# Kernel optimization log

Measured on AMD Instinct MI355X. Metric: run time of the kernel, lower is better.

The kernel has to match this reference:

```python
import jax, jax.numpy as jnp
import numpy as np

D = 4          # subsample stride for quantized refs
R = 6          # local search radius
P = 2 * R + 1  # 13
N = P * P      # 169
C = 32         # one-hot classes
BETA = 50.0
SIG = 1.0      # gaussian kernel sigma for kernel_soft_argmax
MPR = 12       # memory_patch_R
MPP = 2 * MPR + 1  # 25
DIL_INT = 15


def bilinear_gather(img, ys, xs):
    # img (b,c,h,w); ys,xs (b,n,h,w) float pixel coords; zero padding outside.
    b, c, h, w = img.shape
    y0f = jnp.floor(ys); x0f = jnp.floor(xs)
    wy = ys - y0f; wx = xs - x0f
    y0 = y0f.astype(jnp.int32); x0 = x0f.astype(jnp.int32)
    imgf = img.reshape(b, c, h * w)

    def corner(yi, xi, wgt):
        valid = (yi >= 0) & (yi < h) & (xi >= 0) & (xi < w)
        idx = jnp.clip(yi, 0, h - 1) * w + jnp.clip(xi, 0, w - 1)  # (b,n,h,w)
        g = jax.vmap(lambda f, ix: f[:, ix])(imgf, idx)            # (b,c,n,h,w)
        return g * (wgt * valid)[:, None]

    return (corner(y0, x0, (1 - wy) * (1 - wx))
            + corner(y0, x0 + 1, (1 - wy) * wx)
            + corner(y0 + 1, x0, wy * (1 - wx))
            + corner(y0 + 1, x0 + 1, wy * wx))


def deform_im2col(img, offset):
    # img (b,c,h,w); offset (b,h,w,2) ordered (dx,dy); returns (b,c,N,h,w)
    b, c, h, w = img.shape
    n = jnp.arange(N)
    dy = (n // P - R).astype(jnp.float32)
    dx = (n % P - R).astype(jnp.float32)
    yy = jnp.arange(h, dtype=jnp.float32)[:, None]
    xx = jnp.arange(w, dtype=jnp.float32)[None, :]
    ys = yy[None, None] + offset[..., 1][:, None] + dy[None, :, None, None]
    xs = xx[None, None] + offset[..., 0][:, None] + dx[None, :, None, None]
    return bilinear_gather(img, ys, xs)


def local_corr(t, r, rad, dil):
    # SpatialCorrelationSampler(kernel_size=1, patch_size=2*rad+1, dilation_patch=dil)
    pad = rad * dil
    rp = jnp.pad(r, ((0, 0), (0, 0), (pad, pad), (pad, pad)))
    offs = jnp.arange(2 * rad + 1) * dil

    def dot(oy, ox):
        rs = jax.lax.dynamic_slice(rp, (0, 0, oy, ox), t.shape)
        return jnp.sum(t * rs, axis=1)  # (b,h,w)

    f = jax.vmap(lambda oy: jax.vmap(lambda ox: dot(oy, ox))(offs))(offs)  # (Pp,Pp,b,h,w)
    return jnp.transpose(f, (2, 0, 1, 3, 4))  # (b,Pp,Pp,h,w), axis1=dy, axis2=dx


def unfold(x, ksz, pad):
    # torch F.unfold: (b,c,h,w) -> (b,c,ksz*ksz,h*w), n = ky*ksz+kx, zero pad
    b, c, h, w = x.shape
    xp = jnp.pad(x, ((0, 0), (0, 0), (pad, pad), (pad, pad)))
    offs = jnp.arange(ksz)
    sl = jax.vmap(lambda oy: jax.vmap(
        lambda ox: jax.lax.dynamic_slice(xp, (0, 0, oy, ox), x.shape))(offs))(offs)
    return jnp.transpose(sl, (2, 3, 0, 1, 4, 5)).reshape(b, c, ksz * ksz, h * w)


def kernel_soft_argmax(corr):
    # corr (B, N, h, w): gaussian-weight then softmax(beta * .) over N
    k = jnp.arange(P, dtype=jnp.float32)
    ctr = (P - 1) / 2.0
    g = jnp.exp(-(((k[None, :] - ctr) ** 2) + ((k[:, None] - ctr) ** 2)) / (2 * SIG ** 2))
    return jax.nn.softmax(BETA * (g.reshape(1, N, 1, 1) * corr), axis=1)


def get_grid(corr):
    # corr (B, N, h, w) -> soft-argmax grid (B, h, w, 2) in normalized coords
    B, n, h, w = corr.shape
    # replicate the torch meshgrid variable swap in the original get_grid
    x_map = jnp.broadcast_to(jnp.linspace(-1.0, 1.0, w)[None, :], (h, w)).astype(jnp.float32)
    y_map = jnp.broadcast_to(jnp.linspace(-1.0, 1.0, h)[:, None], (h, w)).astype(jnp.float32)
    xg = unfold(x_map[None, None], P, R)[:, 0]  # (1,N,hw)
    yg = unfold(y_map[None, None], P, R)[:, 0]
    wgt = corr.reshape(B, n, h * w)
    wgt = wgt / jnp.sum(wgt, 1, keepdims=True)
    gx = (wgt * xg).sum(1).reshape(B, h, w, 1)
    gy = (wgt * yg).sum(1).reshape(B, h, w, 1)
    return jnp.concatenate([gx, gy], 3)


def forward(feats_r, feats_t, quantized_r, ref_index, current_ind):
    ref_list = [int(v) for v in np.asarray(ref_index)]  # static config
    cur = int(current_ind)
    nref = feats_r.shape[0]
    nsearch = len([x for x in ref_list if cur - x > DIL_INT])
    dirates = [min(4, (cur - x) // DIL_INT + 1) for x in ref_list if cur - x > DIL_INT]
    b, c, h, w = feats_t.shape

    mdy = jnp.arange(-MPR, MPR + 1, dtype=jnp.float32)
    corrs, offsets = [], []
    for si in range(nsearch):
        cc = local_corr(feats_t, feats_r[si], MPR, dirates[si])       # (b,25,25,h,w)
        cc = jax.nn.softmax(cc.reshape(b, MPP * MPP, h * w), axis=1)
        cc = cc.reshape(b, MPP, MPP, h, w)
        offx = jnp.einsum('bpqhw,q->bhw', cc, mdy)   # expectation of dx
        offy = jnp.einsum('bpqhw,p->bhw', cc, mdy)   # expectation of dy
        off = jnp.stack([offx, offy], -1) * float(dirates[si])        # (b,h,w,2)
        offsets.append(off)
        col0 = deform_im2col(feats_r[si], off)                        # (b,c,N,h,w)
        corrs.append(jnp.einsum('bchw,bcnhw->bnhw', feats_t, col0))
    for ind in range(nsearch, nref):
        corrs.append(local_corr(feats_t, feats_r[ind], R, 1).reshape(b, N, h, w))

    corr = jnp.concatenate(corrs, 0)                 # (b*nref, N, h, w)
    corr = kernel_soft_argmax(corr)
    corr = corr.reshape(b, 1, N * nref, h * w)
    grid = get_grid(corr.reshape(-1, N, h, w))       # (b*nref, h, w, 2)

    # prep: subsample ::D and one-hot single-channel label maps
    labels = quantized_r[:, :, 0, ::D, ::D]          # (nref, b, h, w)
    qr = (labels[:, :, None] == jnp.arange(C)[None, None, :, None, None]).astype(jnp.float32)

    cols = []
    for i in range(nsearch):
        cols.append(deform_im2col(qr[i], offsets[i]).reshape(b, C, N, h * w))
    for i in range(nsearch, nref):
        cols.append(unfold(qr[i], P, R))
    image_uf = jnp.concatenate(cols, 2)              # (b, C, N*nref, hw)

    out = jnp.einsum('bnl,bcnl->bcl', corr[:, 0], image_uf).reshape(b, C, h, w)
    return out, grid


def setup_inputs() -> dict:
    key = jax.random.key(0)
    k1, k2, k3 = jax.random.split(key, 3)
    feats_r = jax.random.normal(k1, (3, 1, 64, 64, 64), dtype=jnp.float32)
    feats_t = jax.random.normal(k2, (1, 64, 64, 64), dtype=jnp.float32)
    quantized_r = jax.random.randint(k3, (3, 1, 1, 256, 256), 0, C, dtype=jnp.int32)
    return {
        'feats_r': feats_r,
        'feats_t': feats_t,
        'quantized_r': quantized_r,
        'ref_index': np.arange(3),
        'current_ind': 16,
    }


def reference(feats_r, feats_t, quantized_r, ref_index, current_ind):
    return forward(feats_r, feats_t, quantized_r, ref_index, current_ind)
```

## Files before the change

kernel.cpp:

```cpp
#include <hip/hip_runtime.h>


#define NPIX 4096

typedef float f32x2 __attribute__((ext_vector_type(2)));

__device__ __forceinline__ f32x2 pkfma(f32x2 a, f32x2 b, f32x2 c) {
  f32x2 d;
  asm("v_pk_fma_f32 %0, %1, %2, %3" : "=v"(d) : "v"(a), "v"(b), "v"(c));
  return d;
}

__device__ __forceinline__ f32x2 pdot8p(float4 t0, float4 t1, float4 a,
                                        float4 b, f32x2 acc) {
  f32x2 t0l = {t0.x, t0.y}, t0h = {t0.z, t0.w};
  f32x2 t1l = {t1.x, t1.y}, t1h = {t1.z, t1.w};
  f32x2 al = {a.x, a.y}, ah = {a.z, a.w};
  f32x2 bl = {b.x, b.y}, bh = {b.z, b.w};
  acc = pkfma(t0l, al, acc);
  acc = pkfma(t0h, ah, acc);
  acc = pkfma(t1l, bl, acc);
  acc = pkfma(t1h, bh, acc);
  return acc;
}

__device__ __forceinline__ float red8_8(float p0, float p1, float p2,
                                        float p3, float p4, float p5,
                                        float p6, float p7, int tx) {
  bool o1 = tx & 1, o2 = tx & 2, o4 = tx & 4;
  float a = (o1 ? p1 : p0) + __shfl_xor(o1 ? p0 : p1, 1);
  float b = (o1 ? p3 : p2) + __shfl_xor(o1 ? p2 : p3, 1);
  float c = (o1 ? p5 : p4) + __shfl_xor(o1 ? p4 : p5, 1);
  float d = (o1 ? p7 : p6) + __shfl_xor(o1 ? p6 : p7, 1);
  float e = (o2 ? b : a) + __shfl_xor(o2 ? a : b, 2);
  float f = (o2 ? d : c) + __shfl_xor(o2 ? c : d, 2);
  return (o4 ? f : e) + __shfl_xor(o4 ? e : f, 4);
}

__device__ __forceinline__ float red8(float v) {
  v += __shfl_xor(v, 1);
  v += __shfl_xor(v, 2);
  v += __shfl_xor(v, 4);
  return v;
}

__device__ __forceinline__ float wredmax(float v) {
#pragma unroll
  for (int o = 32; o; o >>= 1) v = fmaxf(v, __shfl_down(v, o));
  return __shfl(v, 0);
}
__device__ __forceinline__ float wredsum(float v) {
#pragma unroll
  for (int o = 32; o; o >>= 1) v += __shfl_down(v, o);
  return __shfl(v, 0);
}

__global__ __launch_bounds__(256) void k_transpose(
    const float* __restrict__ ft, const float* __restrict__ fr,
    const int* __restrict__ q, float* __restrict__ tT, float* __restrict__ rT,
    unsigned char* __restrict__ lblp) {
  __shared__ float tile[64][65];
  int img = blockIdx.y;
  int pixBase = blockIdx.x * 64;
  const float* src = (img == 0) ? ft : fr + (img - 1) * (64 * NPIX);
  float* dst = (img == 0) ? tT : rT + (img - 1) * (64 * NPIX);
  int tid = threadIdx.x;
#pragma unroll
  for (int it = 0; it < 4; ++it) {
    int idx = it * 256 + tid;
    int c = idx >> 4;
    int p4 = (idx & 15) << 2;
    float4 v = *(const float4*)&src[c * NPIX + pixBase + p4];
    tile[p4 + 0][c] = v.x;
    tile[p4 + 1][c] = v.y;
    tile[p4 + 2][c] = v.z;
    tile[p4 + 3][c] = v.w;
  }
  __syncthreads();
#pragma unroll
  for (int it = 0; it < 4; ++it) {
    int idx = it * 256 + tid;
    int p = idx >> 4;
    int c4 = (idx & 15) << 2;
    float4 v = make_float4(tile[p][c4], tile[p][c4 + 1], tile[p][c4 + 2],
                           tile[p][c4 + 3]);
    *(float4*)&dst[(pixBase + p) * 64 + c4] = v;
  }
  if (img >= 1 && tid < 64) {
    int pix = pixBase + tid;
    lblp[(img - 1) * 4096 + pix] = (unsigned char)
        q[(img - 1) * 65536 + (pix >> 6) * 1024 + (pix & 63) * 4];
  }
}

__global__ __launch_bounds__(512, 4) void k_fused(
    const float* __restrict__ tT, const float* __restrict__ rT,
    const unsigned char* __restrict__ lblp, float* __restrict__ out,
    float* __restrict__ grid) {
  int xg = blockIdx.x, y = blockIdx.y;
  int x0 = (xg >> 1) * 16 + (xg & 1);
  int tid = threadIdx.x;
  int g8 = tid >> 3, tx = tid & 7;
  int w = tid >> 6, lane = tid & 63;

  __shared__ float cc1[8 * 636];
  __shared__ float D[8][196];
  __shared__ float P0[8][169];
  __shared__ float cc2[8][169];
  __shared__ float bins[8][33];

  if (tid < 264) ((float*)bins)[tid] = 0.f;

  const f32x2 zz = {0.f, 0.f};

  const float4* tb = (const float4*)&tT[((y << 6) + x0) << 6];
  float4 t0a = tb[0 * 32 + 2 * tx], t0b = tb[0 * 32 + 2 * tx + 1];
  float4 t1a = tb[1 * 32 + 2 * tx], t1b = tb[1 * 32 + 2 * tx + 1];
  float4 t2a = tb[2 * 32 + 2 * tx], t2b = tb[2 * 32 + 2 * tx + 1];
  float4 t3a = tb[3 * 32 + 2 * tx], t3b = tb[3 * 32 + 2 * tx + 1];
  float4 t4a = tb[4 * 32 + 2 * tx], t4b = tb[4 * 32 + 2 * tx + 1];
  float4 t5a = tb[5 * 32 + 2 * tx], t5b = tb[5 * 32 + 2 * tx + 1];
  float4 t6a = tb[6 * 32 + 2 * tx], t6b = tb[6 * 32 + 2 * tx + 1];
  float4 t7a = tb[7 * 32 + 2 * tx], t7b = tb[7 * 32 + 2 * tx + 1];

  {
    int u = g8 & 31, oyb = g8 >> 5;
    int rx = x0 - 24 + 2 * u;
    bool cok = (unsigned)rx < 64u;
    int colB = min(max(rx, 0), 63) * 64 + tx * 8;
    int ox = u - tx;
    bool sok = (unsigned)ox < 25u;
#pragma unroll 4
    for (int r = 0; r < 13; ++r) {
      int oy = oyb + 2 * r;
      int ry = y + 2 * oy - 24;
      bool ok = cok & (oy < 25) & ((unsigned)ry < 64u);
      const float4* rp = (const float4*)&rT[min(max(ry, 0), 63) * 4096 + colB];
      float4 ra = rp[0], rb = rp[1];
      f32x2 a0 = pdot8p(t0a, t0b, ra, rb, zz);
      f32x2 a1 = pdot8p(t1a, t1b, ra, rb, zz);
      f32x2 a2 = pdot8p(t2a, t2b, ra, rb, zz);
      f32x2 a3 = pdot8p(t3a, t3b, ra, rb, zz);
      f32x2 a4 = pdot8p(t4a, t4b, ra, rb, zz);
      f32x2 a5 = pdot8p(t5a, t5b, ra, rb, zz);
      f32x2 a6 = pdot8p(t6a, t6b, ra, rb, zz);
      f32x2 a7 = pdot8p(t7a, t7b, ra, rb, zz);
      float v = red8_8(a0.x + a0.y, a1.x + a1.y, a2.x + a2.y, a3.x + a3.y,
                       a4.x + a4.y, a5.x + a5.y, a6.x + a6.y, a7.x + a7.y,
                       tx);
      v = ok ? v : 0.f;
      if (sok && (oy < 25)) cc1[tx * 636 + oy * 25 + ox] = v;
    }
  }
  __syncthreads();

  float offx, offy;
  {
    float vv[10];
    float m = -3e38f;
#pragma unroll
    for (int it = 0; it < 10; ++it) {
      unsigned o = lane + (it << 6);
      float v = (o < 625u) ? cc1[w * 636 + o] : -3e38f;
      vv[it] = v;
      m = fmaxf(m, v);
    }
    m = wredmax(m);
    float s = 0.f, sx = 0.f, sy = 0.f;
#pragma unroll
    for (int it = 0; it < 10; ++it) {
      unsigned o = lane + (it << 6);
      unsigned oy = o / 25u, ox = o - oy * 25u;
      float e = __expf(vv[it] - m);
      s += e;
      sx += e * (float)((int)ox - 12);
      sy += e * (float)((int)oy - 12);
    }
    s = wredsum(s);
    sx = wredsum(sx);
    sy = wredsum(sy);
    offx = 2.f * sx / s;
    offy = 2.f * sy / s;
  }

  float fy = floorf(offy), fx = floorf(offx);
  float wy = offy - fy, wx = offx - fx;
  float w00 = (1.f - wy) * (1.f - wx), w01 = (1.f - wy) * wx;
  float w10 = wy * (1.f - wx), w11 = wy * wx;
  int iy0 = y + (int)fy - 6;
  int ix0 = x0 + 2 * w + (int)fx - 6;

  {
    const float4* Tp = (const float4*)&tT[((y << 6) + x0 + 2 * w) << 6];
    float4 T0 = Tp[2 * tx], T1 = Tp[2 * tx + 1];
    int g3 = lane >> 3;
#pragma unroll 4
    for (int r = 0; r < 28; ++r) {
      int idx = g3 + (r << 3);
      int a = idx >> 4, b = idx & 15;
      int ry = iy0 + a, rx = ix0 + b;
      bool ok = (b < 14) & ((unsigned)ry < 64u) & ((unsigned)rx < 64u);
      const float4* rp = (const float4*)
          &rT[(min(max(ry, 0), 63) * 64 + min(max(rx, 0), 63)) * 64];
      float4 ra = rp[2 * tx], rb = rp[2 * tx + 1];
      f32x2 acc = pdot8p(T0, T1, ra, rb, zz);
      float v = red8(acc.x + acc.y);
      if (tx == 0 && b < 14) D[w][a * 14 + b] = ok ? v : 0.f;
    }
  }

  {
    int px = x0 + 2 * w, pix = (y << 6) + px;
    float sc[3];
    float m = -3e38f;
#pragma unroll
    for (int it = 0; it < 3; ++it) {
      unsigned o = lane + (it << 6);
      float scv = -3e38f;
      if (o < 169u) {
        unsigned i = o / 13u, j = o - i * 13u;
        float v = w00 * D[w][i * 14 + j] + w01 * D[w][i * 14 + j + 1] +
                  w10 * D[w][(i + 1) * 14 + j] +
                  w11 * D[w][(i + 1) * 14 + j + 1];
        float di = (float)(((int)i - 6) * ((int)i - 6) +
                           ((int)j - 6) * ((int)j - 6));
        scv = 50.f * __expf(-0.5f * di) * v;
      }
      sc[it] = scv;
      m = fmaxf(m, scv);
    }
    m = wredmax(m);
    float ee[3];
    float s = 0.f, gx = 0.f, gy = 0.f;
#pragma unroll
    for (int it = 0; it < 3; ++it) {
      unsigned o = lane + (it << 6);
      unsigned i = o / 13u, j = o - i * 13u;
      float e = __expf(sc[it] - m);
      ee[it] = e;
      int yy = y + (int)i - 6, xx = px + (int)j - 6;
      bool inb = (o < 169u) && (unsigned)yy < 64u && (unsigned)xx < 64u;
      s += e;
      gx += e * (inb ? (-1.f + (2.f / 63.f) * (float)xx) : 0.f);
      gy += e * (inb ? (-1.f + (2.f / 63.f) * (float)yy) : 0.f);
    }
    s = wredsum(s);
    gx = wredsum(gx);
    gy = wredsum(gy);
    float invS = 1.f / s;
#pragma unroll
    for (int it = 0; it < 3; ++it) {
      unsigned o = lane + (it << 6);
      if (o < 169u) P0[w][o] = ee[it] * invS;
    }
    if (lane == 0) {
      grid[pix * 2 + 0] = gx * invS;
      grid[pix * 2 + 1] = gy * invS;
    }
  }

  {
#pragma unroll
    for (int it = 0; it < 4; ++it) {
      int idx = lane + (it << 6);
      int a = idx >> 4, b = idx & 15;
      if (a < 14 && b < 14) {
        int ry = iy0 + a, rx = ix0 + b;
        if ((unsigned)ry < 64u && (unsigned)rx < 64u) {
          float wgt = 0.f;
          const float* crp = P0[w];
          if (a < 13) {
            if (b < 13) wgt = fmaf(w00, crp[a * 13 + b], wgt);
            if (b > 0) wgt = fmaf(w01, crp[a * 13 + b - 1], wgt);
          }
          if (a > 0) {
            if (b < 13) wgt = fmaf(w10, crp[(a - 1) * 13 + b], wgt);
            if (b > 0) wgt = fmaf(w11, crp[(a - 1) * 13 + b - 1], wgt);
          }
          if (wgt != 0.f) atomicAdd(&bins[w][lblp[ry * 64 + rx]], wgt);
        }
      }
    }
  }

#pragma unroll 1
  for (int k = 1; k <= 2; ++k) {
    const float* rb0 = rT + (k << 18);
    __syncthreads();
    {
      int u = g8 & 31, ib = g8 >> 5;
      int rx = x0 - 6 + u;
      bool cok = (unsigned)rx < 64u;
      int colB = min(max(rx, 0), 63) * 64 + tx * 8;
      int j = u - 2 * tx;
      bool sok = (unsigned)j < 13u;
#pragma unroll 4
      for (int r = 0; r < 7; ++r) {
        int i = ib + 2 * r;
        int ry = y + i - 6;
        bool ok = cok & (i < 13) & ((unsigned)ry < 64u);
        const float4* rp =
            (const float4*)&rb0[min(max(ry, 0), 63) * 4096 + colB];
        float4 ra = rp[0], rb = rp[1];
        f32x2 a0 = pdot8p(t0a, t0b, ra, rb, zz);
        f32x2 a1 = pdot8p(t1a, t1b, ra, rb, zz);
        f32x2 a2 = pdot8p(t2a, t2b, ra, rb, zz);
        f32x2 a3 = pdot8p(t3a, t3b, ra, rb, zz);
        f32x2 a4 = pdot8p(t4a, t4b, ra, rb, zz);
        f32x2 a5 = pdot8p(t5a, t5b, ra, rb, zz);
        f32x2 a6 = pdot8p(t6a, t6b, ra, rb, zz);
        f32x2 a7 = pdot8p(t7a, t7b, ra, rb, zz);
        float v = red8_8(a0.x + a0.y, a1.x + a1.y, a2.x + a2.y, a3.x + a3.y,
                         a4.x + a4.y, a5.x + a5.y, a6.x + a6.y, a7.x + a7.y,
                         tx);
        v = ok ? v : 0.f;
        if (sok && (i < 13)) cc2[tx][i * 13 + j] = v;
      }
    }
    __syncthreads();
    {
      int px = x0 + 2 * w, pix = (y << 6) + px;
      float sc[3];
      float m = -3e38f;
#pragma unroll
      for (int it = 0; it < 3; ++it) {
        unsigned o = lane + (it << 6);
        float scv = -3e38f;
        if (o < 169u) {
          unsigned i = o / 13u, j = o - i * 13u;
          float di = (float)(((int)i - 6) * ((int)i - 6) +
                             ((int)j - 6) * ((int)j - 6));
          scv = 50.f * __expf(-0.5f * di) * cc2[w][o];
        }
        sc[it] = scv;
        m = fmaxf(m, scv);
      }
      m = wredmax(m);
      float ee[3];
      float s = 0.f, gx = 0.f, gy = 0.f;
#pragma unroll
      for (int it = 0; it < 3; ++it) {
        unsigned o = lane + (it << 6);
        unsigned i = o / 13u, j = o - i * 13u;
        float e = __expf(sc[it] - m);
        ee[it] = e;
        int yy = y + (int)i - 6, xx = px + (int)j - 6;
        bool inb = (o < 169u) && (unsigned)yy < 64u && (unsigned)xx < 64u;
        s += e;
        gx += e * (inb ? (-1.f + (2.f / 63.f) * (float)xx) : 0.f);
        gy += e * (inb ? (-1.f + (2.f / 63.f) * (float)yy) : 0.f);
      }
      s = wredsum(s);
      gx = wredsum(gx);
      gy = wredsum(gy);
      float invS = 1.f / s;
#pragma unroll
      for (int it = 0; it < 3; ++it) {
        unsigned o = lane + (it << 6);
        if (o < 169u) {
          unsigned i = o / 13u, j = o - i * 13u;
          int yy = y + (int)i - 6, xx = px + (int)j - 6;
          if ((unsigned)yy < 64u && (unsigned)xx < 64u)
            atomicAdd(&bins[w][lblp[(k << 12) + yy * 64 + xx]],
                      ee[it] * invS);
        }
      }
      if (lane == 0) {
        grid[(k * NPIX + pix) * 2 + 0] = gx * invS;
        grid[(k * NPIX + pix) * 2 + 1] = gy * invS;
      }
    }
    __syncthreads();
  }

  if (tid < 256) {
    int pp = tid & 7, c = tid >> 3;
    out[c * NPIX + (y << 6) + x0 + 2 * pp] = bins[pp][c];
  }
}

extern "C" void kernel_launch(void* const* d_in, const int* in_sizes, int n_in,
                              void* d_out, int out_size, void* d_ws,
                              size_t ws_size, hipStream_t stream) {
  const float* fr = (const float*)d_in[0];
  const float* ft = (const float*)d_in[1];
  const int* q = (const int*)d_in[2];
  float* out = (float*)d_out;
  float* grid = out + 32 * NPIX;

  float* ws = (float*)d_ws;
  float* tT = ws;
  float* rT = ws + 262144;
  unsigned char* lblp = (unsigned char*)(ws + 1048576);

  k_transpose<<<dim3(64, 4), 256, 0, stream>>>(ft, fr, q, tT, rT, lblp);
  k_fused<<<dim3(8, 64), 512, 0, stream>>>(tT, rT, lblp, out, grid);
}
```

Measured before the change: 55.40 us.

## Split reference frames across grid z-dimension and merge bins with global atomics

The fused kernel now launches a 3-deep grid in z so that the deformable search frame and the two local-window frames run in separate blocks instead of sequentially inside one block. Per-block class bins are combined with atomicAdd into an output buffer that is zeroed by a memset first. The cc2 buffer now aliases cc1 to cut shared memory, and the packed v_pk_fma inline asm is replaced by plain scalar fmaf dot products. This trades three times the blocks, a memset and global atomics for shorter per-block serial work, at the cost of a load imbalance because the z=0 blocks do more work than the others.

Measured after the change: 61.45 us. +10.9%, slower.

```diff
diff --git a/kernel.cpp b/kernel.cpp
--- a/kernel.cpp
+++ b/kernel.cpp
@@ -3,25 +3,14 @@
 
 #define NPIX 4096
 
-typedef float f32x2 __attribute__((ext_vector_type(2)));
-
-__device__ __forceinline__ f32x2 pkfma(f32x2 a, f32x2 b, f32x2 c) {
-  f32x2 d;
-  asm("v_pk_fma_f32 %0, %1, %2, %3" : "=v"(d) : "v"(a), "v"(b), "v"(c));
-  return d;
-}
-
-__device__ __forceinline__ f32x2 pdot8p(float4 t0, float4 t1, float4 a,
-                                        float4 b, f32x2 acc) {
-  f32x2 t0l = {t0.x, t0.y}, t0h = {t0.z, t0.w};
-  f32x2 t1l = {t1.x, t1.y}, t1h = {t1.z, t1.w};
-  f32x2 al = {a.x, a.y}, ah = {a.z, a.w};
-  f32x2 bl = {b.x, b.y}, bh = {b.z, b.w};
-  acc = pkfma(t0l, al, acc);
-  acc = pkfma(t0h, ah, acc);
-  acc = pkfma(t1l, bl, acc);
-  acc = pkfma(t1h, bh, acc);
-  return acc;
+__device__ __forceinline__ float pdot8(float4 t0, float4 t1, float4 a,
+                                       float4 b) {
+  float s0 = t0.x * a.x, s1 = t0.y * a.y, s2 = t0.z * a.z, s3 = t0.w * a.w;
+  s0 = fmaf(t1.x, b.x, s0);
+  s1 = fmaf(t1.y, b.y, s1);
+  s2 = fmaf(t1.z, b.z, s2);
+  s3 = fmaf(t1.w, b.w, s3);
+  return (s0 + s1) + (s2 + s3);
 }
 
 __device__ __forceinline__ float red8_8(float p0, float p1, float p2,
@@ -97,7 +86,7 @@
     const float* __restrict__ tT, const float* __restrict__ rT,
     const unsigned char* __restrict__ lblp, float* __restrict__ out,
     float* __restrict__ grid) {
-  int xg = blockIdx.x, y = blockIdx.y;
+  int xg = blockIdx.x, y = blockIdx.y, z = blockIdx.z;
   int x0 = (xg >> 1) * 16 + (xg & 1);
   int tid = threadIdx.x;
   int g8 = tid >> 3, tx = tid & 7;
@@ -106,12 +95,9 @@
   __shared__ float cc1[8 * 636];
   __shared__ float D[8][196];
   __shared__ float P0[8][169];
-  __shared__ float cc2[8][169];
   __shared__ float bins[8][33];
 
   if (tid < 264) ((float*)bins)[tid] = 0.f;
-
-  const f32x2 zz = {0.f, 0.f};
 
   const float4* tb = (const float4*)&tT[((y << 6) + x0) << 6];
   float4 t0a = tb[0 * 32 + 2 * tx], t0b = tb[0 * 32 + 2 * tx + 1];
@@ -123,170 +109,165 @@
   float4 t6a = tb[6 * 32 + 2 * tx], t6b = tb[6 * 32 + 2 * tx + 1];
   float4 t7a = tb[7 * 32 + 2 * tx], t7b = tb[7 * 32 + 2 * tx + 1];
 
-  {
-    int u = g8 & 31, oyb = g8 >> 5;
-    int rx = x0 - 24 + 2 * u;
-    bool cok = (unsigned)rx < 64u;
-    int colB = min(max(rx, 0), 63) * 64 + tx * 8;
-    int ox = u - tx;
-    bool sok = (unsigned)ox < 25u;
+  if (z == 0) {
+    {
+      int u = g8 & 31, oyb = g8 >> 5;
+      int rx = x0 - 24 + 2 * u;
+      bool cok = (unsigned)rx < 64u;
+      int colB = min(max(rx, 0), 63) * 64 + tx * 8;
+      int ox = u - tx;
+      bool sok = (unsigned)ox < 25u;
 #pragma unroll 4
-    for (int r = 0; r < 13; ++r) {
-      int oy = oyb + 2 * r;
-      int ry = y + 2 * oy - 24;
-      bool ok = cok & (oy < 25) & ((unsigned)ry < 64u);
-      const float4* rp = (const float4*)&rT[min(max(ry, 0), 63) * 4096 + colB];
-      float4 ra = rp[0], rb = rp[1];
-      f32x2 a0 = pdot8p(t0a, t0b, ra, rb, zz);
-      f32x2 a1 = pdot8p(t1a, t1b, ra, rb, zz);
-      f32x2 a2 = pdot8p(t2a, t2b, ra, rb, zz);
-      f32x2 a3 = pdot8p(t3a, t3b, ra, rb, zz);
-      f32x2 a4 = pdot8p(t4a, t4b, ra, rb, zz);
-      f32x2 a5 = pdot8p(t5a, t5b, ra, rb, zz);
-      f32x2 a6 = pdot8p(t6a, t6b, ra, rb, zz);
-      f32x2 a7 = pdot8p(t7a, t7b, ra, rb, zz);
-      float v = red8_8(a0.x + a0.y, a1.x + a1.y, a2.x + a2.y, a3.x + a3.y,
-                       a4.x + a4.y, a5.x + a5.y, a6.x + a6.y, a7.x + a7.y,
-                       tx);
-      v = ok ? v : 0.f;
-      if (sok && (oy < 25)) cc1[tx * 636 + oy * 25 + ox] = v;
-    }
-  }
-  __syncthreads();
-
-  float offx, offy;
-  {
-    float vv[10];
-    float m = -3e38f;
-#pragma unroll
-    for (int it = 0; it < 10; ++it) {
-      unsigned o = lane + (it << 6);
-      float v = (o < 625u) ? cc1[w * 636 + o] : -3e38f;
-      vv[it] = v;
-      m = fmaxf(m, v);
-    }
-    m = wredmax(m);
-    float s = 0.f, sx = 0.f, sy = 0.f;
-#pragma unroll
-    for (int it = 0; it < 10; ++it) {
-      unsigned o = lane + (it << 6);
-      unsigned oy = o / 25u, ox = o - oy * 25u;
-      float e = __expf(vv[it] - m);
-      s += e;
-      sx += e * (float)((int)ox - 12);
-      sy += e * (float)((int)oy - 12);
-    }
-    s = wredsum(s);
-    sx = wredsum(sx);
-    sy = wredsum(sy);
-    offx = 2.f * sx / s;
-    offy = 2.f * sy / s;
-  }
-
-  float fy = floorf(offy), fx = floorf(offx);
-  float wy = offy - fy, wx = offx - fx;
-  float w00 = (1.f - wy) * (1.f - wx), w01 = (1.f - wy) * wx;
-  float w10 = wy * (1.f - wx), w11 = wy * wx;
-  int iy0 = y + (int)fy - 6;
-  int ix0 = x0 + 2 * w + (int)fx - 6;
-
-  {
-    const float4* Tp = (const float4*)&tT[((y << 6) + x0 + 2 * w) << 6];
-    float4 T0 = Tp[2 * tx], T1 = Tp[2 * tx + 1];
-    int g3 = lane >> 3;
+      for (int r = 0; r < 13; ++r) {
+        int oy = oyb + 2 * r;
+        int ry = y + 2 * oy - 24;
+        bool ok = cok & (oy < 25) & ((unsigned)ry < 64u);
+        const float4* rp =
+            (const float4*)&rT[min(max(ry, 0), 63) * 4096 + colB];
+        float4 ra = rp[0], rb = rp[1];
+        float v = red8_8(pdot8(t0a, t0b, ra, rb), pdot8(t1a, t1b, ra, rb),
+                         pdot8(t2a, t2b, ra, rb), pdot8(t3a, t3b, ra, rb),
+                         pdot8(t4a, t4b, ra, rb), pdot8(t5a, t5b, ra, rb),
+                         pdot8(t6a, t6b, ra, rb), pdot8(t7a, t7b, ra, rb),
+                         tx);
+        v = ok ? v : 0.f;
+        if (sok && (oy < 25)) cc1[tx * 636 + oy * 25 + ox] = v;
+      }
+    }
+    __syncthreads();
+
+    float offx, offy;
+    {
+      float vv[10];
+      float m = -3e38f;
+#pragma unroll
+      for (int it = 0; it < 10; ++it) {
+        unsigned o = lane + (it << 6);
+        float v = (o < 625u) ? cc1[w * 636 + o] : -3e38f;
+        vv[it] = v;
+        m = fmaxf(m, v);
+      }
+      m = wredmax(m);
+      float s = 0.f, sx = 0.f, sy = 0.f;
+#pragma unroll
+      for (int it = 0; it < 10; ++it) {
+        unsigned o = lane + (it << 6);
+        unsigned oy = o / 25u, ox = o - oy * 25u;
+        float e = __expf(vv[it] - m);
+        s += e;
+        sx += e * (float)((int)ox - 12);
+        sy += e * (float)((int)oy - 12);
+      }
+      s = wredsum(s);
+      sx = wredsum(sx);
+      sy = wredsum(sy);
+      offx = 2.f * sx / s;
+      offy = 2.f * sy / s;
+    }
+
+    float fy = floorf(offy), fx = floorf(offx);
+    float wy = offy - fy, wx = offx - fx;
+    float w00 = (1.f - wy) * (1.f - wx), w01 = (1.f - wy) * wx;
+    float w10 = wy * (1.f - wx), w11 = wy * wx;
+    int iy0 = y + (int)fy - 6;
+    int ix0 = x0 + 2 * w + (int)fx - 6;
+
+    {
+      const float4* Tp = (const float4*)&tT[((y << 6) + x0 + 2 * w) << 6];
+      float4 T0 = Tp[2 * tx], T1 = Tp[2 * tx + 1];
+      int g3 = lane >> 3;
 #pragma unroll 4
-    for (int r = 0; r < 28; ++r) {
-      int idx = g3 + (r << 3);
-      int a = idx >> 4, b = idx & 15;
-      int ry = iy0 + a, rx = ix0 + b;
-      bool ok = (b < 14) & ((unsigned)ry < 64u) & ((unsigned)rx < 64u);
-      const float4* rp = (const float4*)
-          &rT[(min(max(ry, 0), 63) * 64 + min(max(rx, 0), 63)) * 64];
-      float4 ra = rp[2 * tx], rb = rp[2 * tx + 1];
-      f32x2 acc = pdot8p(T0, T1, ra, rb, zz);
-      float v = red8(acc.x + acc.y);
-      if (tx == 0 && b < 14) D[w][a * 14 + b] = ok ? v : 0.f;
-    }
-  }
-
-  {
-    int px = x0 + 2 * w, pix = (y << 6) + px;
-    float sc[3];
-    float m = -3e38f;
-#pragma unroll
-    for (int it = 0; it < 3; ++it) {
-      unsigned o = lane + (it << 6);
-      float scv = -3e38f;
-      if (o < 169u) {
+      for (int r = 0; r < 28; ++r) {
+        int idx = g3 + (r << 3);
+        int a = idx >> 4, b = idx & 15;
+        int ry = iy0 + a, rx = ix0 + b;
+        bool ok = (b < 14) & ((unsigned)ry < 64u) & ((unsigned)rx < 64u);
+        const float4* rp = (const float4*)
+            &rT[(min(max(ry, 0), 63) * 64 + min(max(rx, 0), 63)) * 64];
+        float4 ra = rp[2 * tx], rb = rp[2 * tx + 1];
+        float v = red8(pdot8(T0, T1, ra, rb));
+        if (tx == 0 && b < 14) D[w][a * 14 + b] = ok ? v : 0.f;
+      }
+    }
+
+    {
+      int px = x0 + 2 * w, pix = (y << 6) + px;
+      float sc[3];
+      float m = -3e38f;
+#pragma unroll
+      for (int it = 0; it < 3; ++it) {
+        unsigned o = lane + (it << 6);
+        float scv = -3e38f;
+        if (o < 169u) {
+          unsigned i = o / 13u, j = o - i * 13u;
+          float v = w00 * D[w][i * 14 + j] + w01 * D[w][i * 14 + j + 1] +
+                    w10 * D[w][(i + 1) * 14 + j] +
+                    w11 * D[w][(i + 1) * 14 + j + 1];
+          float di = (float)(((int)i - 6) * ((int)i - 6) +
+                             ((int)j - 6) * ((int)j - 6));
+          scv = 50.f * __expf(-0.5f * di) * v;
+        }
+        sc[it] = scv;
+        m = fmaxf(m, scv);
+      }
+      m = wredmax(m);
+      float ee[3];
+      float s = 0.f, gx = 0.f, gy = 0.f;
+#pragma unroll
+      for (int it = 0; it < 3; ++it) {
+        unsigned o = lane + (it << 6);
         unsigned i = o / 13u, j = o - i * 13u;
-        float v = w00 * D[w][i * 14 + j] + w01 * D[w][i * 14 + j + 1] +
-                  w10 * D[w][(i + 1) * 14 + j] +
-                  w11 * D[w][(i + 1) * 14 + j + 1];
-        float di = (float)(((int)i - 6) * ((int)i - 6) +
-                           ((int)j - 6) * ((int)j - 6));
-        scv = 50.f * __expf(-0.5f * di) * v;
-      }
-      sc[it] = scv;
-      m = fmaxf(m, scv);
-    }
-    m = wredmax(m);
-    float ee[3];
-    float s = 0.f, gx = 0.f, gy = 0.f;
-#pragma unroll
-    for (int it = 0; it < 3; ++it) {
-      unsigned o = lane + (it << 6);
-      unsigned i = o / 13u, j = o - i * 13u;
-      float e = __expf(sc[it] - m);
-      ee[it] = e;
-      int yy = y + (int)i - 6, xx = px + (int)j - 6;
-      bool inb = (o < 169u) && (unsigned)yy < 64u && (unsigned)xx < 64u;
-      s += e;
-      gx += e * (inb ? (-1.f + (2.f / 63.f) * (float)xx) : 0.f);
-      gy += e * (inb ? (-1.f + (2.f / 63.f) * (float)yy) : 0.f);
-    }
-    s = wredsum(s);
-    gx = wredsum(gx);
-    gy = wredsum(gy);
-    float invS = 1.f / s;
-#pragma unroll
-    for (int it = 0; it < 3; ++it) {
-      unsigned o = lane + (it << 6);
-      if (o < 169u) P0[w][o] = ee[it] * invS;
-    }
-    if (lane == 0) {
-      grid[pix * 2 + 0] = gx * invS;
-      grid[pix * 2 + 1] = gy * invS;
-    }
-  }
-
-  {
-#pragma unroll
-    for (int it = 0; it < 4; ++it) {
-      int idx = lane + (it << 6);
-      int a = idx >> 4, b = idx & 15;
-      if (a < 14 && b < 14) {
-        int ry = iy0 + a, rx = ix0 + b;
-        if ((unsigned)ry < 64u && (unsigned)rx < 64u) {
-          float wgt = 0.f;
-          const float* crp = P0[w];
-          if (a < 13) {
-            if (b < 13) wgt = fmaf(w00, crp[a * 13 + b], wgt);
-            if (b > 0) wgt = fmaf(w01, crp[a * 13 + b - 1], wgt);
+        float e = __expf(sc[it] - m);
+        ee[it] = e;
+        int yy = y + (int)i - 6, xx = px + (int)j - 6;
+        bool inb = (o < 169u) && (unsigned)yy < 64u && (unsigned)xx < 64u;
+        s += e;
+        gx += e * (inb ? (-1.f + (2.f / 63.f) * (float)xx) : 0.f);
+        gy += e * (inb ? (-1.f + (2.f / 63.f) * (float)yy) : 0.f);
+      }
+      s = wredsum(s);
+      gx = wredsum(gx);
+      gy = wredsum(gy);
+      float invS = 1.f / s;
+#pragma unroll
+      for (int it = 0; it < 3; ++it) {
+        unsigned o = lane + (it << 6);
+        if (o < 169u) P0[w][o] = ee[it] * invS;
+      }
+      if (lane == 0) {
+        grid[pix * 2 + 0] = gx * invS;
+        grid[pix * 2 + 1] = gy * invS;
+      }
+    }
+
+    {
+#pragma unroll
+      for (int it = 0; it < 4; ++it) {
+        int idx = lane + (it << 6);
+        int a = idx >> 4, b = idx & 15;
+        if (a < 14 && b < 14) {
+          int ry = iy0 + a, rx = ix0 + b;
+          if ((unsigned)ry < 64u && (unsigned)rx < 64u) {
+            float wgt = 0.f;
+            const float* crp = P0[w];
+            if (a < 13) {
+              if (b < 13) wgt = fmaf(w00, crp[a * 13 + b], wgt);
+              if (b > 0) wgt = fmaf(w01, crp[a * 13 + b - 1], wgt);
+            }
+            if (a > 0) {
+              if (b < 13) wgt = fmaf(w10, crp[(a - 1) * 13 + b], wgt);
+              if (b > 0) wgt = fmaf(w11, crp[(a - 1) * 13 + b - 1], wgt);
+            }
+            if (wgt != 0.f) atomicAdd(&bins[w][lblp[ry * 64 + rx]], wgt);
           }
-          if (a > 0) {
-            if (b < 13) wgt = fmaf(w10, crp[(a - 1) * 13 + b], wgt);
-            if (b > 0) wgt = fmaf(w11, crp[(a - 1) * 13 + b - 1], wgt);
-          }
-          if (wgt != 0.f) atomicAdd(&bins[w][lblp[ry * 64 + rx]], wgt);
         }
       }
     }
-  }
-
-#pragma unroll 1
-  for (int k = 1; k <= 2; ++k) {
+    __syncthreads();
+  } else {
+    int k = z;
     const float* rb0 = rT + (k << 18);
-    __syncthreads();
+    float (*cc2)[169] = (float(*)[169])cc1;
     {
       int u = g8 & 31, ib = g8 >> 5;
       int rx = x0 - 6 + u;
@@ -302,16 +283,10 @@
         const float4* rp =
             (const float4*)&rb0[min(max(ry, 0), 63) * 4096 + colB];
         float4 ra = rp[0], rb = rp[1];
-        f32x2 a0 = pdot8p(t0a, t0b, ra, rb, zz);
-        f32x2 a1 = pdot8p(t1a, t1b, ra, rb, zz);
-        f32x2 a2 = pdot8p(t2a, t2b, ra, rb, zz);
-        f32x2 a3 = pdot8p(t3a, t3b, ra, rb, zz);
-        f32x2 a4 = pdot8p(t4a, t4b, ra, rb, zz);
-        f32x2 a5 = pdot8p(t5a, t5b, ra, rb, zz);
-        f32x2 a6 = pdot8p(t6a, t6b, ra, rb, zz);
-        f32x2 a7 = pdot8p(t7a, t7b, ra, rb, zz);
-        float v = red8_8(a0.x + a0.y, a1.x + a1.y, a2.x + a2.y, a3.x + a3.y,
-                         a4.x + a4.y, a5.x + a5.y, a6.x + a6.y, a7.x + a7.y,
+        float v = red8_8(pdot8(t0a, t0b, ra, rb), pdot8(t1a, t1b, ra, rb),
+                         pdot8(t2a, t2b, ra, rb), pdot8(t3a, t3b, ra, rb),
+                         pdot8(t4a, t4b, ra, rb), pdot8(t5a, t5b, ra, rb),
+                         pdot8(t6a, t6b, ra, rb), pdot8(t7a, t7b, ra, rb),
                          tx);
         v = ok ? v : 0.f;
         if (sok && (i < 13)) cc2[tx][i * 13 + j] = v;
@@ -375,7 +350,7 @@
 
   if (tid < 256) {
     int pp = tid & 7, c = tid >> 3;
-    out[c * NPIX + (y << 6) + x0 + 2 * pp] = bins[pp][c];
+    atomicAdd(&out[c * NPIX + (y << 6) + x0 + 2 * pp], bins[pp][c]);
   }
 }
 
@@ -393,6 +368,7 @@
   float* rT = ws + 262144;
   unsigned char* lblp = (unsigned char*)(ws + 1048576);
 
+  hipMemsetAsync(out, 0, 32 * NPIX * sizeof(float), stream);
   k_transpose<<<dim3(64, 4), 256, 0, stream>>>(ft, fr, q, tT, rT, lblp);
-  k_fused<<<dim3(8, 64), 512, 0, stream>>>(tT, rT, lblp, out, grid);
-}
+  k_fused<<<dim3(8, 64, 3), 512, 0, stream>>>(tT, rT, lblp, out, grid);
+}
```
